# Optimization experiments

Hardware: AMD Instinct MI355X
Metric: run time of the kernel (lower is better)

Reference implementation:

```python
import jax, jax.numpy as jnp
import numpy as np

TOP_K = 4  # moe_top_k


def setup_inputs() -> dict:
    key = jax.random.key(0)
    k1, k2 = jax.random.split(key)
    # hidden states [B, S, D]
    x = jax.random.normal(k1, (4, 4096, 6144), dtype=jnp.float32)
    # router weight [D, E] (nnx.Linear kernel, no bias)
    W = jax.random.normal(k2, (6144, 16), dtype=jnp.float32) * 0.02
    return {"x": x, "W": W}


def reference(x, W):
    # logits: [B, S, E] -- promote to fp32 as the module does
    logits = jnp.einsum('bsd,de->bse', x.astype(jnp.float32), W.astype(jnp.float32))
    weights = jax.nn.softmax(logits, axis=-1)
    # top-k expert selection
    top_weights, top_experts = jax.lax.top_k(weights, TOP_K)
    # moe_normalize_expert_weights = 1 -> L1 normalize the selected weights
    top_weights = top_weights / jnp.sum(jnp.abs(top_weights), axis=-1, keepdims=True)
    return (weights.astype(x.dtype), top_weights.astype(x.dtype), top_experts)
```

## Files before the change

kernel.cpp:

```cpp
#include <hip/hip_runtime.h>
#include <cmath>


namespace {
constexpr int TOKENS = 16384;
constexpr int DIM    = 6144;
constexpr int NE     = 16;
constexpr int TOPK   = 4;
constexpr int T_TILE = 64;
constexpr int SUPER  = 256;
constexpr int RS     = 258;
constexpr int RPAD   = 20;
constexpr int KSL    = 4;
constexpr int NTILES = TOKENS / T_TILE;
constexpr int TOPW_OFF = TOKENS * NE;
constexpr int EXP_OFF  = TOPW_OFF + TOKENS * TOPK;
}

__device__ __forceinline__ void fma16(float xs, const float* __restrict__ wrow,
                                      float (&ac)[NE]) {
    const float4 w0 = *reinterpret_cast<const float4*>(wrow + 0);
    const float4 w1 = *reinterpret_cast<const float4*>(wrow + 4);
    const float4 w2 = *reinterpret_cast<const float4*>(wrow + 8);
    const float4 w3 = *reinterpret_cast<const float4*>(wrow + 12);
    ac[0]  = fmaf(xs, w0.x, ac[0]);  ac[1]  = fmaf(xs, w0.y, ac[1]);
    ac[2]  = fmaf(xs, w0.z, ac[2]);  ac[3]  = fmaf(xs, w0.w, ac[3]);
    ac[4]  = fmaf(xs, w1.x, ac[4]);  ac[5]  = fmaf(xs, w1.y, ac[5]);
    ac[6]  = fmaf(xs, w1.z, ac[6]);  ac[7]  = fmaf(xs, w1.w, ac[7]);
    ac[8]  = fmaf(xs, w2.x, ac[8]);  ac[9]  = fmaf(xs, w2.y, ac[9]);
    ac[10] = fmaf(xs, w2.z, ac[10]); ac[11] = fmaf(xs, w2.w, ac[11]);
    ac[12] = fmaf(xs, w3.x, ac[12]); ac[13] = fmaf(xs, w3.y, ac[13]);
    ac[14] = fmaf(xs, w3.z, ac[14]); ac[15] = fmaf(xs, w3.w, ac[15]);
}

__global__ __launch_bounds__(512) void router_partial_kernel(
    const float* __restrict__ x, const float* __restrict__ W,
    float* __restrict__ partial)
{
    constexpr int KS = DIM / KSL;
    constexpr int NS = KS / SUPER;

    __shared__ float smem[T_TILE * RS];

    const int tid  = threadIdx.x;
    const int lane = tid & 63;
    const int wv   = tid >> 6;
    const int wvu  = __builtin_amdgcn_readfirstlane(wv);
    const int slice = blockIdx.x & 3;
    const int tile  = blockIdx.x >> 2;
    const int t0 = tile * T_TILE;
    const int d0 = slice * KS;

    const float* xb = x + (size_t)(t0 + wv) * DIM + d0 + lane * 4;

    float acc[NE];
    #pragma unroll
    for (int e = 0; e < NE; ++e) acc[e] = 0.f;

    float4 buf[8];
    #pragma unroll
    for (int i = 0; i < 8; ++i)
        buf[i] = *reinterpret_cast<const float4*>(xb + (size_t)(i * 8) * DIM);

    #pragma unroll 1
    for (int s = 0; s < NS; ++s) {
        #pragma unroll
        for (int i = 0; i < 8; ++i) {
            float* dst = &smem[(size_t)(i * 8 + wv) * RS + lane * 4];
            *reinterpret_cast<float2*>(dst)     = make_float2(buf[i].x, buf[i].y);
            *reinterpret_cast<float2*>(dst + 2) = make_float2(buf[i].z, buf[i].w);
        }
        if (s + 1 < NS) {
            const float* xn = xb + (size_t)(s + 1) * SUPER;
            #pragma unroll
            for (int i = 0; i < 8; ++i)
                buf[i] = *reinterpret_cast<const float4*>(xn + (size_t)(i * 8) * DIM);
        }
        __syncthreads();
        {
            const float* xr = &smem[(size_t)lane * RS + wvu * 32];
            const float* wp = W + (size_t)(d0 + s * SUPER + wvu * 32) * NE;
            #pragma unroll
            for (int q = 0; q < 16; ++q) {
                const float2 xq = *reinterpret_cast<const float2*>(xr + 2 * q);
                fma16(xq.x, wp + (2 * q) * NE, acc);
                fma16(xq.y, wp + (2 * q + 1) * NE, acc);
            }
        }
        __syncthreads();
    }

    #pragma unroll
    for (int q = 0; q < 4; ++q)
        *reinterpret_cast<float4*>(&smem[(size_t)(wvu * 64 + lane) * RPAD + 4 * q]) =
            make_float4(acc[4 * q], acc[4 * q + 1], acc[4 * q + 2], acc[4 * q + 3]);
    __syncthreads();

    if (wv == 0) {
        float4 r0[4];
        #pragma unroll
        for (int q = 0; q < 4; ++q)
            r0[q] = *reinterpret_cast<const float4*>(&smem[(size_t)lane * RPAD + 4 * q]);
        #pragma unroll
        for (int w = 1; w < 8; ++w) {
            #pragma unroll
            for (int q = 0; q < 4; ++q) {
                const float4 rw = *reinterpret_cast<const float4*>(
                    &smem[(size_t)(w * 64 + lane) * RPAD + 4 * q]);
                r0[q].x += rw.x; r0[q].y += rw.y; r0[q].z += rw.z; r0[q].w += rw.w;
            }
        }
        float* p = partial + ((size_t)slice * TOKENS + t0 + lane) * NE;
        #pragma unroll
        for (int q = 0; q < 4; ++q)
            *reinterpret_cast<float4*>(p + 4 * q) = r0[q];
    }
}

__global__ __launch_bounds__(128) void router_finish_kernel(
    const float* __restrict__ partial, float* __restrict__ out)
{
    const int t = blockIdx.x * 128 + threadIdx.x;
    float l[NE];
    {
        const float4* p0 = reinterpret_cast<const float4*>(partial + (size_t)t * NE);
        float4 a0 = p0[0], a1 = p0[1], a2 = p0[2], a3 = p0[3];
        #pragma unroll
        for (int s = 1; s < KSL; ++s) {
            const float4* q = reinterpret_cast<const float4*>(
                partial + ((size_t)s * TOKENS + t) * NE);
            float4 b0 = q[0], b1 = q[1], b2 = q[2], b3 = q[3];
            a0.x += b0.x; a0.y += b0.y; a0.z += b0.z; a0.w += b0.w;
            a1.x += b1.x; a1.y += b1.y; a1.z += b1.z; a1.w += b1.w;
            a2.x += b2.x; a2.y += b2.y; a2.z += b2.z; a2.w += b2.w;
            a3.x += b3.x; a3.y += b3.y; a3.z += b3.z; a3.w += b3.w;
        }
        l[0]=a0.x; l[1]=a0.y; l[2]=a0.z; l[3]=a0.w;
        l[4]=a1.x; l[5]=a1.y; l[6]=a1.z; l[7]=a1.w;
        l[8]=a2.x; l[9]=a2.y; l[10]=a2.z; l[11]=a2.w;
        l[12]=a3.x; l[13]=a3.y; l[14]=a3.z; l[15]=a3.w;
    }
    float mx = l[0];
    #pragma unroll
    for (int e = 1; e < NE; ++e) mx = fmaxf(mx, l[e]);
    float w[NE];
    float sum = 0.f;
    #pragma unroll
    for (int e = 0; e < NE; ++e) { w[e] = expf(l[e] - mx); sum += w[e]; }
    const float inv = 1.f / sum;
    #pragma unroll
    for (int e = 0; e < NE; ++e) w[e] *= inv;

    int   idx[TOPK];
    float tw[TOPK];
    unsigned used = 0;
    #pragma unroll
    for (int k = 0; k < TOPK; ++k) {
        float best = -1.f;
        int   bi   = 0;
        #pragma unroll
        for (int e = 0; e < NE; ++e) {
            const bool avail = ((used >> e) & 1u) == 0u;
            if (avail && w[e] > best) { best = w[e]; bi = e; }
        }
        used |= (1u << bi);
        idx[k] = bi;
        tw[k]  = best;
    }
    const float s4 = tw[0] + tw[1] + tw[2] + tw[3];
    const float rinv = 1.f / s4;

    float4* o0 = reinterpret_cast<float4*>(out + (size_t)t * NE);
    o0[0] = make_float4(w[0], w[1], w[2], w[3]);
    o0[1] = make_float4(w[4], w[5], w[6], w[7]);
    o0[2] = make_float4(w[8], w[9], w[10], w[11]);
    o0[3] = make_float4(w[12], w[13], w[14], w[15]);
    *reinterpret_cast<float4*>(out + TOPW_OFF + (size_t)t * TOPK) =
        make_float4(tw[0] * rinv, tw[1] * rinv, tw[2] * rinv, tw[3] * rinv);
    *reinterpret_cast<float4*>(out + EXP_OFF + (size_t)t * TOPK) =
        make_float4((float)idx[0], (float)idx[1], (float)idx[2], (float)idx[3]);
}

extern "C" void kernel_launch(void* const* d_in, const int* in_sizes, int n_in,
                              void* d_out, int out_size, void* d_ws, size_t ws_size,
                              hipStream_t stream) {
    const float* x = (const float*)d_in[0];
    const float* W = (const float*)d_in[1];
    float* out = (float*)d_out;
    float* ws  = (float*)d_ws;

    router_partial_kernel<<<NTILES * KSL, 512, 0, stream>>>(x, W, ws);
    router_finish_kernel<<<TOKENS / 128, 128, 0, stream>>>(ws, out);
}
```

Before: 96.75 us.

## Fuse router partial and finish kernels via cooperative grid sync

Replaces the two-kernel launch with one cooperative kernel. Each slice-0 block keeps its partial logits in registers, waits on a grid-wide barrier, then reads the other three slices' partials and runs softmax and top-k in place. This removes the second launch and one partial write and read per token. Blocks shrink to 256 threads with a 128-column super-tile to fit four blocks per CU, which is needed for the cooperative launch to hold all 1024 blocks at once. The cost is a grid-wide barrier and a serialized tail done by only a quarter of the blocks; if the cooperative launch fails, it falls back to the two-kernel path.

```diff
diff --git a/kernel.cpp b/kernel.cpp
--- a/kernel.cpp
+++ b/kernel.cpp
@@ -1,5 +1,8 @@
 #include <hip/hip_runtime.h>
+#include <hip/hip_cooperative_groups.h>
 #include <cmath>
+
+namespace cg = cooperative_groups;
 
 
 namespace {
@@ -8,8 +11,8 @@
 constexpr int NE     = 16;
 constexpr int TOPK   = 4;
 constexpr int T_TILE = 64;
-constexpr int SUPER  = 256;
-constexpr int RS     = 258;
+constexpr int SUPER  = 128;
+constexpr int RS     = 130;
 constexpr int RPAD   = 20;
 constexpr int KSL    = 4;
 constexpr int NTILES = TOKENS / T_TILE;
@@ -33,25 +36,68 @@
     ac[14] = fmaf(xs, w3.z, ac[14]); ac[15] = fmaf(xs, w3.w, ac[15]);
 }
 
-__global__ __launch_bounds__(512) void router_partial_kernel(
+__device__ __forceinline__ void finish_token(const float (&l)[NE], int tt,
+                                             float* __restrict__ out) {
+    float mx = l[0];
+    #pragma unroll
+    for (int e = 1; e < NE; ++e) mx = fmaxf(mx, l[e]);
+    float w[NE];
+    float sum = 0.f;
+    #pragma unroll
+    for (int e = 0; e < NE; ++e) { w[e] = expf(l[e] - mx); sum += w[e]; }
+    const float inv = 1.f / sum;
+    #pragma unroll
+    for (int e = 0; e < NE; ++e) w[e] *= inv;
+
+    int   idx[TOPK];
+    float tw[TOPK];
+    unsigned used = 0;
+    #pragma unroll
+    for (int k = 0; k < TOPK; ++k) {
+        float best = -1.f;
+        int   bi   = 0;
+        #pragma unroll
+        for (int e = 0; e < NE; ++e) {
+            const bool avail = ((used >> e) & 1u) == 0u;
+            if (avail && w[e] > best) { best = w[e]; bi = e; }
+        }
+        used |= (1u << bi);
+        idx[k] = bi;
+        tw[k]  = best;
+    }
+    const float s4 = tw[0] + tw[1] + tw[2] + tw[3];
+    const float rinv = 1.f / s4;
+
+    float4* o0 = reinterpret_cast<float4*>(out + (size_t)tt * NE);
+    o0[0] = make_float4(w[0], w[1], w[2], w[3]);
+    o0[1] = make_float4(w[4], w[5], w[6], w[7]);
+    o0[2] = make_float4(w[8], w[9], w[10], w[11]);
+    o0[3] = make_float4(w[12], w[13], w[14], w[15]);
+    *reinterpret_cast<float4*>(out + TOPW_OFF + (size_t)tt * TOPK) =
+        make_float4(tw[0] * rinv, tw[1] * rinv, tw[2] * rinv, tw[3] * rinv);
+    *reinterpret_cast<float4*>(out + EXP_OFF + (size_t)tt * TOPK) =
+        make_float4((float)idx[0], (float)idx[1], (float)idx[2], (float)idx[3]);
+}
+
+template <bool COOP>
+__device__ __forceinline__ void partial_body(
     const float* __restrict__ x, const float* __restrict__ W,
-    float* __restrict__ partial)
+    float* __restrict__ partial, float (&smem)[T_TILE * RS],
+    int slice, int tile, float4 (&r0)[4], bool& have_r0)
 {
     constexpr int KS = DIM / KSL;
     constexpr int NS = KS / SUPER;
-
-    __shared__ float smem[T_TILE * RS];
 
     const int tid  = threadIdx.x;
     const int lane = tid & 63;
     const int wv   = tid >> 6;
     const int wvu  = __builtin_amdgcn_readfirstlane(wv);
-    const int slice = blockIdx.x & 3;
-    const int tile  = blockIdx.x >> 2;
     const int t0 = tile * T_TILE;
     const int d0 = slice * KS;
 
-    const float* xb = x + (size_t)(t0 + wv) * DIM + d0 + lane * 4;
+    const int srow = wv * 2 + (lane >> 5);
+    const int scol = (lane & 31) * 4;
+    const float* xb = x + (size_t)(t0 + srow) * DIM + d0 + scol;
 
     float acc[NE];
     #pragma unroll
@@ -66,7 +112,7 @@
     for (int s = 0; s < NS; ++s) {
         #pragma unroll
         for (int i = 0; i < 8; ++i) {
-            float* dst = &smem[(size_t)(i * 8 + wv) * RS + lane * 4];
+            float* dst = &smem[(size_t)(srow + i * 8) * RS + scol];
             *reinterpret_cast<float2*>(dst)     = make_float2(buf[i].x, buf[i].y);
             *reinterpret_cast<float2*>(dst + 2) = make_float2(buf[i].z, buf[i].w);
         }
@@ -96,13 +142,13 @@
             make_float4(acc[4 * q], acc[4 * q + 1], acc[4 * q + 2], acc[4 * q + 3]);
     __syncthreads();
 
+    have_r0 = false;
     if (wv == 0) {
-        float4 r0[4];
         #pragma unroll
         for (int q = 0; q < 4; ++q)
             r0[q] = *reinterpret_cast<const float4*>(&smem[(size_t)lane * RPAD + 4 * q]);
         #pragma unroll
-        for (int w = 1; w < 8; ++w) {
+        for (int w = 1; w < 4; ++w) {
             #pragma unroll
             for (int q = 0; q < 4; ++q) {
                 const float4 rw = *reinterpret_cast<const float4*>(
@@ -110,11 +156,63 @@
                 r0[q].x += rw.x; r0[q].y += rw.y; r0[q].z += rw.z; r0[q].w += rw.w;
             }
         }
-        float* p = partial + ((size_t)slice * TOKENS + t0 + lane) * NE;
-        #pragma unroll
-        for (int q = 0; q < 4; ++q)
-            *reinterpret_cast<float4*>(p + 4 * q) = r0[q];
-    }
+        have_r0 = true;
+        if (!COOP || slice != 0) {
+            const int sidx = COOP ? (slice - 1) : slice;
+            float* p = partial + ((size_t)sidx * TOKENS + t0 * 1 + lane) * NE
+                       + (size_t)tile * 0;
+            p = partial + ((size_t)sidx * TOKENS + tile * T_TILE + lane) * NE;
+            #pragma unroll
+            for (int q = 0; q < 4; ++q)
+                *reinterpret_cast<float4*>(p + 4 * q) = r0[q];
+        }
+    }
+}
+
+__global__ __launch_bounds__(256, 4) void router_coop_kernel(
+    const float* __restrict__ x, const float* __restrict__ W,
+    float* __restrict__ partial, float* __restrict__ out)
+{
+    __shared__ float smem[T_TILE * RS];
+    const int slice = blockIdx.x % KSL;
+    const int tile  = blockIdx.x / KSL;
+
+    float4 r0[4];
+    bool have_r0;
+    partial_body<true>(x, W, partial, smem, slice, tile, r0, have_r0);
+
+    cg::this_grid().sync();
+
+    if (slice == 0 && have_r0) {
+        const int lane = threadIdx.x & 63;
+        const int t = tile * T_TILE + lane;
+        float4 a0 = r0[0], a1 = r0[1], a2 = r0[2], a3 = r0[3];
+        #pragma unroll
+        for (int s = 0; s < KSL - 1; ++s) {
+            const float4* q = reinterpret_cast<const float4*>(
+                partial + ((size_t)s * TOKENS + t) * NE);
+            float4 b0 = q[0], b1 = q[1], b2 = q[2], b3 = q[3];
+            a0.x += b0.x; a0.y += b0.y; a0.z += b0.z; a0.w += b0.w;
+            a1.x += b1.x; a1.y += b1.y; a1.z += b1.z; a1.w += b1.w;
+            a2.x += b2.x; a2.y += b2.y; a2.z += b2.z; a2.w += b2.w;
+            a3.x += b3.x; a3.y += b3.y; a3.z += b3.z; a3.w += b3.w;
+        }
+        float l[NE] = {a0.x,a0.y,a0.z,a0.w, a1.x,a1.y,a1.z,a1.w,
+                       a2.x,a2.y,a2.z,a2.w, a3.x,a3.y,a3.z,a3.w};
+        finish_token(l, t, out);
+    }
+}
+
+__global__ __launch_bounds__(256) void router_partial_kernel(
+    const float* __restrict__ x, const float* __restrict__ W,
+    float* __restrict__ partial)
+{
+    __shared__ float smem[T_TILE * RS];
+    const int slice = blockIdx.x % KSL;
+    const int tile  = blockIdx.x / KSL;
+    float4 r0[4];
+    bool have_r0;
+    partial_body<false>(x, W, partial, smem, slice, tile, r0, have_r0);
 }
 
 __global__ __launch_bounds__(128) void router_finish_kernel(
@@ -140,45 +238,7 @@
         l[8]=a2.x; l[9]=a2.y; l[10]=a2.z; l[11]=a2.w;
         l[12]=a3.x; l[13]=a3.y; l[14]=a3.z; l[15]=a3.w;
     }
-    float mx = l[0];
-    #pragma unroll
-    for (int e = 1; e < NE; ++e) mx = fmaxf(mx, l[e]);
-    float w[NE];
-    float sum = 0.f;
-    #pragma unroll
-    for (int e = 0; e < NE; ++e) { w[e] = expf(l[e] - mx); sum += w[e]; }
-    const float inv = 1.f / sum;
-    #pragma unroll
-    for (int e = 0; e < NE; ++e) w[e] *= inv;
-
-    int   idx[TOPK];
-    float tw[TOPK];
-    unsigned used = 0;
-    #pragma unroll
-    for (int k = 0; k < TOPK; ++k) {
-        float best = -1.f;
-        int   bi   = 0;
-        #pragma unroll
-        for (int e = 0; e < NE; ++e) {
-            const bool avail = ((used >> e) & 1u) == 0u;
-            if (avail && w[e] > best) { best = w[e]; bi = e; }
-        }
-        used |= (1u << bi);
-        idx[k] = bi;
-        tw[k]  = best;
-    }
-    const float s4 = tw[0] + tw[1] + tw[2] + tw[3];
-    const float rinv = 1.f / s4;
-
-    float4* o0 = reinterpret_cast<float4*>(out + (size_t)t * NE);
-    o0[0] = make_float4(w[0], w[1], w[2], w[3]);
-    o0[1] = make_float4(w[4], w[5], w[6], w[7]);
-    o0[2] = make_float4(w[8], w[9], w[10], w[11]);
-    o0[3] = make_float4(w[12], w[13], w[14], w[15]);
-    *reinterpret_cast<float4*>(out + TOPW_OFF + (size_t)t * TOPK) =
-        make_float4(tw[0] * rinv, tw[1] * rinv, tw[2] * rinv, tw[3] * rinv);
-    *reinterpret_cast<float4*>(out + EXP_OFF + (size_t)t * TOPK) =
-        make_float4((float)idx[0], (float)idx[1], (float)idx[2], (float)idx[3]);
+    finish_token(l, t, out);
 }
 
 extern "C" void kernel_launch(void* const* d_in, const int* in_sizes, int n_in,
@@ -189,6 +249,13 @@
     float* out = (float*)d_out;
     float* ws  = (float*)d_ws;
 
-    router_partial_kernel<<<NTILES * KSL, 512, 0, stream>>>(x, W, ws);
-    router_finish_kernel<<<TOKENS / 128, 128, 0, stream>>>(ws, out);
-}
+    void* args[] = {(void*)&x, (void*)&W, (void*)&ws, (void*)&out};
+    hipError_t err = hipLaunchCooperativeKernel(
+        reinterpret_cast<const void*>(router_coop_kernel),
+        dim3(NTILES * KSL), dim3(256), args, 0, stream);
+
+    if (err != hipSuccess) {
+        router_partial_kernel<<<NTILES * KSL, 256, 0, stream>>>(x, W, ws);
+        router_finish_kernel<<<TOKENS / 128, 128, 0, stream>>>(ws, out);
+    }
+}
```

After: 187.4 us. 1.94x slower.
